# Kernel tuning notes

Hardware: AMD Instinct MI355X
Metric: run time of the kernel (lower is better)

The kernel has to match this reference:

```python
import jax, jax.numpy as jnp
import numpy as np

MIN_SIZE = 16.0
PH, PW, SCALE = 7, 7, 0.0625


def _context_anchor(rois, hh, hw):
    """rois: [N,5] (batch_idx,x1,y1,x2,y2). Returns [N*8,5] context boxes, col0 = 0 label."""
    N = rois.shape[0]
    x1, y1, x2, y2 = rois[:, 1], rois[:, 2], rois[:, 3], rois[:, 4]
    w, h = x2 - x1, y2 - y1
    k = jnp.arange(3, dtype=rois.dtype)
    sx = x1[:, None] + w[:, None] * (k - 0.5)  # x1 - w + w*k + w/2
    sy = y1[:, None] + h[:, None] * (k - 0.5)
    # np.meshgrid(shift_x, shift_y).ravel() is y-major
    cx = jnp.broadcast_to(sx[:, None, :], (N, 3, 3)).reshape(N, 9)
    cy = jnp.broadcast_to(sy[:, :, None], (N, 3, 3)).reshape(N, 9)
    boxes = jnp.stack([cx - w[:, None] / 4, cy - h[:, None] / 4,
                       cx + w[:, None] / 4, cy + h[:, None] / 4], -1)  # [N,9,4]
    bw = boxes[..., 2] - boxes[..., 0] + 1
    bh = boxes[..., 3] - boxes[..., 1] + 1
    invalid = ((boxes[..., 0] < 0) | (boxes[..., 1] < 0) |
               (boxes[..., 2] >= hw) | (boxes[..., 3] >= hh) |
               (bw < MIN_SIZE) | (bh < MIN_SIZE))
    boxes = jnp.where(invalid[..., None], rois[:, None, 1:5], boxes)
    boxes = boxes[:, jnp.array([0, 1, 2, 3, 5, 6, 7, 8]), :]  # drop center cell
    gt = boxes.reshape(N * 8, 4)  # K = 8N
    # IoU(all roi boxes, gt) with +1 pixel convention (bbox_overlaps_batch)
    A = rois[:, 1:5]
    aw, ah = A[:, 2] - A[:, 0] + 1, A[:, 3] - A[:, 1] + 1
    gw, gh = gt[:, 2] - gt[:, 0] + 1, gt[:, 3] - gt[:, 1] + 1
    iw = jnp.maximum(jnp.minimum(A[:, None, 2], gt[None, :, 2]) - jnp.maximum(A[:, None, 0], gt[None, :, 0]) + 1, 0)
    ih = jnp.maximum(jnp.minimum(A[:, None, 3], gt[None, :, 3]) - jnp.maximum(A[:, None, 1], gt[None, :, 1]) + 1, 0)
    inter = iw * ih
    ov = inter / ((aw * ah)[:, None] + (gw * gh)[None, :] - inter)  # [N,K]
    ov = jnp.where(((gw == 1) & (gh == 1))[None, :], 0.0, ov)
    ov = jnp.where(((aw == 1) & (ah == 1))[:, None], -1.0, ov)
    gt_max = ov.max(0)          # best overlap per gt box
    best = ov.argmax(0)         # index of best-matching roi (torch's `_`)
    labels = gt_max >= 0.3
    w_cell, h_cell = gt[:, 2] - gt[:, 0], gt[:, 3] - gt[:, 1]
    rw = jnp.where(labels, rois[best, 3] - rois[best, 1], 0.0)
    rh = jnp.where(labels, rois[best, 4] - rois[best, 2], 0.0)
    labels = (labels & ~(jnp.maximum(rw, rh) >= jnp.maximum(w_cell, h_cell))
                     & ~(jnp.minimum(rw, rh) < jnp.minimum(w_cell, h_cell) / 3))
    gt = jnp.where(labels[:, None], rois[best][:, 1:5], gt)
    # original zeroes labels at the end -> label column is all zeros
    return jnp.concatenate([jnp.zeros((N * 8, 1), rois.dtype), gt], -1)


def _roi_pool(features, boxes, ph, pw, scale):
    """Classic Caffe max RoIPool. Assumes batch_size==1 (all batch indices 0)."""
    _, C, H, W = features.shape
    f = features[0]  # [C,H,W]
    sw = jnp.round(boxes[:, 1] * scale)
    sh = jnp.round(boxes[:, 2] * scale)
    ew = jnp.round(boxes[:, 3] * scale)
    eh = jnp.round(boxes[:, 4] * scale)
    bsh = jnp.maximum(eh - sh + 1, 1.0) / ph
    bsw = jnp.maximum(ew - sw + 1, 1.0) / pw
    ii = jnp.arange(ph, dtype=f.dtype)
    jj = jnp.arange(pw, dtype=f.dtype)
    hs = jnp.clip(jnp.floor(ii[None, :] * bsh[:, None]) + sh[:, None], 0, H)   # [R,ph]
    he = jnp.clip(jnp.ceil((ii[None, :] + 1) * bsh[:, None]) + sh[:, None], 0, H)
    ws = jnp.clip(jnp.floor(jj[None, :] * bsw[:, None]) + sw[:, None], 0, W)   # [R,pw]
    we = jnp.clip(jnp.ceil((jj[None, :] + 1) * bsw[:, None]) + sw[:, None], 0, W)
    hidx = jnp.arange(H, dtype=f.dtype)
    widx = jnp.arange(W, dtype=f.dtype)
    mask_h = (hidx >= hs[..., None]) & (hidx < he[..., None])  # [R,ph,H]
    mask_w = (widx >= ws[..., None]) & (widx < we[..., None])  # [R,pw,W]
    NEG = jnp.asarray(-1e30, f.dtype)
    # separable masked max: reduce W per pw-bin, then H per ph-bin
    colmax = jnp.stack([jnp.where(mask_w[:, j, None, None, :], f[None], NEG).max(-1)
                        for j in range(pw)], axis=1)           # [R,pw,C,H]
    out = jnp.stack([jnp.where(mask_h[:, i, None, None, :], colmax, NEG).max(-1)
                     for i in range(ph)], axis=1)              # [R,ph,pw,C]
    valid = mask_h.any(-1)[:, :, None] & mask_w.any(-1)[:, None, :]
    out = jnp.where(valid[..., None], out, 0.0)                # empty bins -> 0
    return jnp.transpose(out, (0, 3, 1, 2))                    # [R,C,ph,pw]


def reference(features, rois, hh, hw):
    N = rois.shape[0]
    gt = _context_anchor(rois, hh, hw).reshape(N, 8, 5)
    cat_rois = jnp.concatenate([rois[:, None, :], gt], 1).reshape(-1, 5)  # [9N,5]
    pool = _roi_pool(features, cat_rois, PH, PW, SCALE)                   # [9N,C,7,7]
    pool_feat = pool.reshape(N, -1, PW, PH)                               # [N,9C,7,7]
    return pool_feat, cat_rois


def setup_inputs() -> dict:
    key = jax.random.key(0)
    k1, k2, k3, k4, k5 = jax.random.split(key, 5)
    N, C, Hf, Wf, IMG = 32, 256, 40, 40, 640
    x1 = jax.random.uniform(k1, (N,), minval=0.0, maxval=IMG - 220.0)
    y1 = jax.random.uniform(k2, (N,), minval=0.0, maxval=IMG - 220.0)
    bw = jax.random.uniform(k3, (N,), minval=80.0, maxval=200.0)
    bh = jax.random.uniform(k4, (N,), minval=80.0, maxval=200.0)
    rois = jnp.stack([jnp.zeros((N,)), x1, y1, x1 + bw, y1 + bh], -1).astype(jnp.float32)
    features = jax.random.normal(k5, (1, C, Hf, Wf), dtype=jnp.float32)
    return {"features": features, "rois": rois, "hh": 640, "hw": 640}
```

## Files before the change

### kernel.cpp

```cpp
#include <hip/hip_runtime.h>
#include <math.h>

#define N_ROIS   32
#define N_CAT    (N_ROIS * 9)
#define C_FEAT   256
#define H_FEAT   40
#define W_FEAT   40
#define P_FEAT   (H_FEAT * W_FEAT)
#define PH       7
#define PW       7
#define SCALE    0.0625f
#define MIN_SIZE 16.0f
#define CELLS    (PH * PW)
#define POOL_PER_BOX (C_FEAT * CELLS)
#define OUT_POOL_ELEMS ((size_t)N_CAT * POOL_PER_BOX)

#define N_TRANS_BLOCKS (P_FEAT / 32 * (C_FEAT / 32))
#define WIN 14

__global__ void prep_kernel(const float* __restrict__ f,
                            const float* __restrict__ rois,
                            const int* __restrict__ hh_p,
                            const int* __restrict__ hw_p,
                            float* __restrict__ ft,
                            float* __restrict__ cat_out,
                            int use_transpose) {
    __shared__ float tile[32][33];
    __shared__ float R[N_ROIS * 5];
    const int bid = blockIdx.x;
    const int tid = threadIdx.x;

    if (bid < N_TRANS_BLOCKS) {
        if (!use_transpose) return;
        const int pt = (bid % (P_FEAT / 32)) * 32;
        const int ct = (bid / (P_FEAT / 32)) * 32;
        const int lx = tid & 31;
        const int ly = tid >> 5;
        #pragma unroll
        for (int i = 0; i < 32; i += 8)
            tile[ly + i][lx] = f[(ct + ly + i) * P_FEAT + (pt + lx)];
        __syncthreads();
        #pragma unroll
        for (int i = 0; i < 32; i += 8)
            ft[(pt + ly + i) * C_FEAT + (ct + lx)] = tile[lx][ly + i];
        return;
    }

    if (tid < N_ROIS * 5) R[tid] = rois[tid];
    __syncthreads();

    const float hh = (float)(*hh_p);
    const float hw = (float)(*hw_p);

    const int g = tid;
    const int n = g >> 3;
    const int j = g & 7;
    const int m = (j < 4) ? j : j + 1;
    const int r  = m / 3;
    const int cc = m % 3;

    const float x1 = R[n * 5 + 1], y1 = R[n * 5 + 2];
    const float x2 = R[n * 5 + 3], y2 = R[n * 5 + 4];
    const float w = x2 - x1, h = y2 - y1;

    const float cx = x1 + w * ((float)cc - 0.5f);
    const float cy = y1 + h * ((float)r  - 0.5f);
    float bx1 = cx - w * 0.25f;
    float by1 = cy - h * 0.25f;
    float bx2 = cx + w * 0.25f;
    float by2 = cy + h * 0.25f;
    const float bw = bx2 - bx1 + 1.0f;
    const float bh = by2 - by1 + 1.0f;
    const bool invalid = (bx1 < 0.0f) || (by1 < 0.0f) ||
                         (bx2 >= hw) || (by2 >= hh) ||
                         (bw < MIN_SIZE) || (bh < MIN_SIZE);
    if (invalid) { bx1 = x1; by1 = y1; bx2 = x2; by2 = y2; }

    const float gw = bx2 - bx1 + 1.0f;
    const float gh = by2 - by1 + 1.0f;
    const float garea = gw * gh;
    const bool gdeg = (gw == 1.0f) && (gh == 1.0f);

    float best_ov = -INFINITY;
    int best = 0;
    for (int a = 0; a < N_ROIS; ++a) {
        const float ax1 = R[a * 5 + 1], ay1 = R[a * 5 + 2];
        const float ax2 = R[a * 5 + 3], ay2 = R[a * 5 + 4];
        const float aw = ax2 - ax1 + 1.0f, ah = ay2 - ay1 + 1.0f;
        float iw = fminf(ax2, bx2) - fmaxf(ax1, bx1) + 1.0f;
        float ih = fminf(ay2, by2) - fmaxf(ay1, by1) + 1.0f;
        iw = fmaxf(iw, 0.0f);
        ih = fmaxf(ih, 0.0f);
        const float inter = iw * ih;
        float ov = inter / (aw * ah + garea - inter);
        if (gdeg) ov = 0.0f;
        if (aw == 1.0f && ah == 1.0f) ov = -1.0f;
        if (ov > best_ov) { best_ov = ov; best = a; }
    }

    bool label = (best_ov >= 0.3f);
    const float w_cell = bx2 - bx1;
    const float h_cell = by2 - by1;
    const float rw = label ? (R[best * 5 + 3] - R[best * 5 + 1]) : 0.0f;
    const float rh = label ? (R[best * 5 + 4] - R[best * 5 + 2]) : 0.0f;
    label = label &&
            !(fmaxf(rw, rh) >= fmaxf(w_cell, h_cell)) &&
            !(fminf(rw, rh) < fminf(w_cell, h_cell) / 3.0f);
    if (label) {
        bx1 = R[best * 5 + 1]; by1 = R[best * 5 + 2];
        bx2 = R[best * 5 + 3]; by2 = R[best * 5 + 4];
    }

    float* row = cat_out + (size_t)(n * 9 + 1 + j) * 5;
    row[0] = 0.0f;
    row[1] = bx1; row[2] = by1; row[3] = bx2; row[4] = by2;
    if (j == 0) {
        float* rr = cat_out + (size_t)(n * 9) * 5;
        #pragma unroll
        for (int t = 0; t < 5; ++t) rr[t] = R[n * 5 + t];
    }
}

__global__ __launch_bounds__(256) void
roi_pool_kernel(const float* __restrict__ feat,
                const float* __restrict__ cat_rois,
                float* __restrict__ out) {
    const int i = blockIdx.x / N_CAT;
    const int b = blockIdx.x % N_CAT;
    const int c = threadIdx.x;

    const float* cr = cat_rois + (size_t)b * 5;
    const float x1 = cr[1], y1 = cr[2], x2 = cr[3], y2 = cr[4];
    const float sw = rintf(x1 * SCALE);
    const float sh = rintf(y1 * SCALE);
    const float ew = rintf(x2 * SCALE);
    const float eh = rintf(y2 * SCALE);
    const float bsh = fmaxf(eh - sh + 1.0f, 1.0f) * (1.0f / (float)PH);
    const float bsw = fmaxf(ew - sw + 1.0f, 1.0f) * (1.0f / (float)PW);

    const int hs = (int)fminf(fmaxf(floorf((float)i * bsh) + sh, 0.0f), (float)H_FEAT);
    const int he = (int)fminf(fmaxf(ceilf((float)(i + 1) * bsh) + sh, 0.0f), (float)H_FEAT);

    int ws[PW], we[PW];
    #pragma unroll
    for (int j = 0; j < PW; ++j) {
        ws[j] = (int)fminf(fmaxf(floorf((float)j * bsw) + sw, 0.0f), (float)W_FEAT);
        we[j] = (int)fminf(fmaxf(ceilf((float)(j + 1) * bsw) + sw, 0.0f), (float)W_FEAT);
    }

    const int xs = ws[0];
    const bool narrow = (bsw <= 2.0f);

    float mx[PW];
    #pragma unroll
    for (int j = 0; j < PW; ++j) mx[j] = -1e30f;

    if (narrow) {
        for (int y = hs; y < he; ++y) {
            const float* fr = feat + (size_t)(y * W_FEAT) * C_FEAT + c;
            float win[WIN];
            #pragma unroll
            for (int k = 0; k < WIN; ++k) {
                int x = xs + k;
                x = (x < W_FEAT - 1) ? x : (W_FEAT - 1);
                win[k] = fr[(size_t)x * C_FEAT];
            }
            #pragma unroll
            for (int j = 0; j < PW; ++j) {
                const int lo = ws[j], hi = we[j];
                const int kmax = (2 * j + 2 < WIN) ? (2 * j + 2) : WIN;
                #pragma unroll
                for (int k = 0; k < kmax; ++k) {
                    const int x = xs + k;
                    const bool in = (x >= lo) & (x < hi);
                    const float t = fmaxf(mx[j], win[k]);
                    mx[j] = in ? t : mx[j];
                }
            }
        }
    } else {
        for (int y = hs; y < he; ++y) {
            const float* fr = feat + (size_t)(y * W_FEAT) * C_FEAT + c;
            #pragma unroll
            for (int j = 0; j < PW; ++j)
                for (int x = ws[j]; x < we[j]; ++x)
                    mx[j] = fmaxf(mx[j], fr[(size_t)x * C_FEAT]);
        }
    }

    const bool rowv = (he > hs);
    float* ob = out + (size_t)b * POOL_PER_BOX + (size_t)c * CELLS + i * PW;
    #pragma unroll
    for (int j = 0; j < PW; ++j)
        ob[j] = (rowv && (we[j] > ws[j])) ? mx[j] : 0.0f;
}

__global__ __launch_bounds__(256) void
roi_pool_kernel_nchw(const float* __restrict__ feat,
                     const float* __restrict__ cat_rois,
                     float* __restrict__ out) {
    const int i = blockIdx.x / N_CAT;
    const int b = blockIdx.x % N_CAT;
    const int c = threadIdx.x;

    const float* cr = cat_rois + (size_t)b * 5;
    const float sw = rintf(cr[1] * SCALE);
    const float sh = rintf(cr[2] * SCALE);
    const float ew = rintf(cr[3] * SCALE);
    const float eh = rintf(cr[4] * SCALE);
    const float bsh = fmaxf(eh - sh + 1.0f, 1.0f) * (1.0f / (float)PH);
    const float bsw = fmaxf(ew - sw + 1.0f, 1.0f) * (1.0f / (float)PW);

    const int hs = (int)fminf(fmaxf(floorf((float)i * bsh) + sh, 0.0f), (float)H_FEAT);
    const int he = (int)fminf(fmaxf(ceilf((float)(i + 1) * bsh) + sh, 0.0f), (float)H_FEAT);
    int ws[PW], we[PW];
    #pragma unroll
    for (int j = 0; j < PW; ++j) {
        ws[j] = (int)fminf(fmaxf(floorf((float)j * bsw) + sw, 0.0f), (float)W_FEAT);
        we[j] = (int)fminf(fmaxf(ceilf((float)(j + 1) * bsw) + sw, 0.0f), (float)W_FEAT);
    }
    float mx[PW];
    #pragma unroll
    for (int j = 0; j < PW; ++j) mx[j] = -1e30f;
    for (int y = hs; y < he; ++y) {
        const float* fr = feat + (size_t)c * P_FEAT + y * W_FEAT;
        #pragma unroll
        for (int j = 0; j < PW; ++j)
            for (int x = ws[j]; x < we[j]; ++x)
                mx[j] = fmaxf(mx[j], fr[x]);
    }
    const bool rowv = (he > hs);
    float* ob = out + (size_t)b * POOL_PER_BOX + (size_t)c * CELLS + i * PW;
    #pragma unroll
    for (int j = 0; j < PW; ++j)
        ob[j] = (rowv && (we[j] > ws[j])) ? mx[j] : 0.0f;
}

extern "C" void kernel_launch(void* const* d_in, const int* in_sizes, int n_in,
                              void* d_out, int out_size, void* d_ws, size_t ws_size,
                              hipStream_t stream) {
    const float* features = (const float*)d_in[0];
    const float* rois     = (const float*)d_in[1];
    const int*   hh_p     = (const int*)d_in[2];
    const int*   hw_p     = (const int*)d_in[3];

    float* out      = (float*)d_out;
    float* cat_out  = out + OUT_POOL_ELEMS;
    float* ft       = (float*)d_ws;

    const size_t ft_bytes = (size_t)C_FEAT * P_FEAT * sizeof(float);
    const int use_transpose = (ws_size >= ft_bytes) ? 1 : 0;

    hipLaunchKernelGGL(prep_kernel, dim3(N_TRANS_BLOCKS + 1), dim3(256), 0, stream,
                       features, rois, hh_p, hw_p, ft, cat_out, use_transpose);

    if (use_transpose) {
        hipLaunchKernelGGL(roi_pool_kernel, dim3(PH * N_CAT), dim3(C_FEAT), 0, stream,
                           ft, cat_out, out);
    } else {
        hipLaunchKernelGGL(roi_pool_kernel_nchw, dim3(PH * N_CAT), dim3(C_FEAT), 0, stream,
                           features, cat_out, out);
    }
}
```

Before: 82.17 us.

## Pool whole box per block with shared-memory staging for coalesced float4 output

```diff
diff --git a/kernel.cpp b/kernel.cpp
--- a/kernel.cpp
+++ b/kernel.cpp
@@ -17,6 +17,10 @@
 
 #define N_TRANS_BLOCKS (P_FEAT / 32 * (C_FEAT / 32))
 #define WIN 14
+
+#define CH_HALF   128
+#define POOL_BLKS (N_CAT * 2)
+#define HALF_ELEMS (CH_HALF * CELLS)
 
 __global__ void prep_kernel(const float* __restrict__ f,
                             const float* __restrict__ rois,
@@ -121,13 +125,19 @@
     }
 }
 
-__global__ __launch_bounds__(256) void
-roi_pool_kernel(const float* __restrict__ feat,
+__global__ __launch_bounds__(512, 4) void
+pool_box_kernel(const float* __restrict__ feat,
                 const float* __restrict__ cat_rois,
                 float* __restrict__ out) {
-    const int i = blockIdx.x / N_CAT;
-    const int b = blockIdx.x % N_CAT;
-    const int c = threadIdx.x;
+    __shared__ __align__(16) float obuf[HALF_ELEMS];
+
+    const int s     = (blockIdx.x & 7) * (POOL_BLKS / 8) + (blockIdx.x >> 3);
+    const int b     = s >> 1;
+    const int chalf = s & 1;
+    const int tid   = threadIdx.x;
+    const int cl    = tid & (CH_HALF - 1);
+    const int c     = chalf * CH_HALF + cl;
+    const int iq    = tid >> 7;
 
     const float* cr = cat_rois + (size_t)b * 5;
     const float x1 = cr[1], y1 = cr[2], x2 = cr[3], y2 = cr[4];
@@ -138,9 +148,6 @@
     const float bsh = fmaxf(eh - sh + 1.0f, 1.0f) * (1.0f / (float)PH);
     const float bsw = fmaxf(ew - sw + 1.0f, 1.0f) * (1.0f / (float)PW);
 
-    const int hs = (int)fminf(fmaxf(floorf((float)i * bsh) + sh, 0.0f), (float)H_FEAT);
-    const int he = (int)fminf(fmaxf(ceilf((float)(i + 1) * bsh) + sh, 0.0f), (float)H_FEAT);
-
     int ws[PW], we[PW];
     #pragma unroll
     for (int j = 0; j < PW; ++j) {
@@ -151,48 +158,65 @@
     const int xs = ws[0];
     const bool narrow = (bsw <= 2.0f);
 
-    float mx[PW];
-    #pragma unroll
-    for (int j = 0; j < PW; ++j) mx[j] = -1e30f;
-
-    if (narrow) {
-        for (int y = hs; y < he; ++y) {
-            const float* fr = feat + (size_t)(y * W_FEAT) * C_FEAT + c;
-            float win[WIN];
-            #pragma unroll
-            for (int k = 0; k < WIN; ++k) {
-                int x = xs + k;
-                x = (x < W_FEAT - 1) ? x : (W_FEAT - 1);
-                win[k] = fr[(size_t)x * C_FEAT];
-            }
-            #pragma unroll
-            for (int j = 0; j < PW; ++j) {
-                const int lo = ws[j], hi = we[j];
-                const int kmax = (2 * j + 2 < WIN) ? (2 * j + 2) : WIN;
+    #pragma unroll
+    for (int ii = 0; ii < 2; ++ii) {
+        const int i = iq + ii * 4;
+        if (i >= PH) break;
+
+        const int hs = (int)fminf(fmaxf(floorf((float)i * bsh) + sh, 0.0f), (float)H_FEAT);
+        const int he = (int)fminf(fmaxf(ceilf((float)(i + 1) * bsh) + sh, 0.0f), (float)H_FEAT);
+
+        float mx[PW];
+        #pragma unroll
+        for (int j = 0; j < PW; ++j) mx[j] = -1e30f;
+
+        if (narrow) {
+            for (int y = hs; y < he; ++y) {
+                const float* fr = feat + (size_t)(y * W_FEAT) * C_FEAT + c;
+                float win[WIN];
                 #pragma unroll
-                for (int k = 0; k < kmax; ++k) {
-                    const int x = xs + k;
-                    const bool in = (x >= lo) & (x < hi);
-                    const float t = fmaxf(mx[j], win[k]);
-                    mx[j] = in ? t : mx[j];
+                for (int k = 0; k < WIN; ++k) {
+                    int x = xs + k;
+                    x = (x < W_FEAT - 1) ? x : (W_FEAT - 1);
+                    win[k] = fr[(size_t)x * C_FEAT];
+                }
+                #pragma unroll
+                for (int j = 0; j < PW; ++j) {
+                    const int lo = ws[j], hi = we[j];
+                    const int kmax = (2 * j + 2 < WIN) ? (2 * j + 2) : WIN;
+                    #pragma unroll
+                    for (int k = 0; k < kmax; ++k) {
+                        const int x = xs + k;
+                        const bool in = (x >= lo) & (x < hi);
+                        const float t = fmaxf(mx[j], win[k]);
+                        mx[j] = in ? t : mx[j];
+                    }
                 }
             }
+        } else {
+            for (int y = hs; y < he; ++y) {
+                const float* fr = feat + (size_t)(y * W_FEAT) * C_FEAT + c;
+                #pragma unroll
+                for (int j = 0; j < PW; ++j)
+                    for (int x = ws[j]; x < we[j]; ++x)
+                        mx[j] = fmaxf(mx[j], fr[(size_t)x * C_FEAT]);
+            }
         }
-    } else {
-        for (int y = hs; y < he; ++y) {
-            const float* fr = feat + (size_t)(y * W_FEAT) * C_FEAT + c;
-            #pragma unroll
-            for (int j = 0; j < PW; ++j)
-                for (int x = ws[j]; x < we[j]; ++x)
-                    mx[j] = fmaxf(mx[j], fr[(size_t)x * C_FEAT]);
-        }
-    }
-
-    const bool rowv = (he > hs);
-    float* ob = out + (size_t)b * POOL_PER_BOX + (size_t)c * CELLS + i * PW;
-    #pragma unroll
-    for (int j = 0; j < PW; ++j)
-        ob[j] = (rowv && (we[j] > ws[j])) ? mx[j] : 0.0f;
+
+        const bool rowv = (he > hs);
+        float* orow = obuf + cl * CELLS + i * PW;
+        #pragma unroll
+        for (int j = 0; j < PW; ++j)
+            orow[j] = (rowv && (we[j] > ws[j])) ? mx[j] : 0.0f;
+    }
+
+    __syncthreads();
+
+    const float4* src = reinterpret_cast<const float4*>(obuf);
+    float4* dst = reinterpret_cast<float4*>(out + (size_t)b * POOL_PER_BOX
+                                                + (size_t)chalf * HALF_ELEMS);
+    for (int e = tid; e < HALF_ELEMS / 4; e += 512)
+        dst[e] = src[e];
 }
 
 __global__ __launch_bounds__(256) void
@@ -255,7 +279,7 @@
                        features, rois, hh_p, hw_p, ft, cat_out, use_transpose);
 
     if (use_transpose) {
-        hipLaunchKernelGGL(roi_pool_kernel, dim3(PH * N_CAT), dim3(C_FEAT), 0, stream,
+        hipLaunchKernelGGL(pool_box_kernel, dim3(POOL_BLKS), dim3(512), 0, stream,
                            ft, cat_out, out);
     } else {
         hipLaunchKernelGGL(roi_pool_kernel_nchw, dim3(PH * N_CAT), dim3(C_FEAT), 0, stream,
```

New measurement: 86.12 us. 4.8% more time.

## Fuse anchor prep and ROI pooling into one kernel with shared-memory window

Applied to the files above, without the earlier changes.

```diff
diff --git a/kernel.cpp b/kernel.cpp
--- a/kernel.cpp
+++ b/kernel.cpp
@@ -15,176 +15,183 @@
 #define POOL_PER_BOX (C_FEAT * CELLS)
 #define OUT_POOL_ELEMS ((size_t)N_CAT * POOL_PER_BOX)
 
-#define N_TRANS_BLOCKS (P_FEAT / 32 * (C_FEAT / 32))
-#define WIN 14
-
-__global__ void prep_kernel(const float* __restrict__ f,
-                            const float* __restrict__ rois,
-                            const int* __restrict__ hh_p,
-                            const int* __restrict__ hw_p,
-                            float* __restrict__ ft,
-                            float* __restrict__ cat_out,
-                            int use_transpose) {
-    __shared__ float tile[32][33];
+#define CH_G      64
+#define NCHG      (C_FEAT / CH_G)
+#define POOL_BLKS (N_CAT * NCHG)
+#define THREADS   448
+#define WROWS     14
+#define WCOLS     14
+#define WSTRIDE   197
+
+__global__ __launch_bounds__(THREADS, 4) void
+fused_pool_kernel(const float* __restrict__ f,
+                  const float* __restrict__ rois,
+                  const int* __restrict__ hh_p,
+                  const int* __restrict__ hw_p,
+                  float* __restrict__ out) {
     __shared__ float R[N_ROIS * 5];
+    __shared__ float BX[4];
+    __shared__ __align__(16) float win[CH_G * WSTRIDE];
+
     const int bid = blockIdx.x;
+    const int s   = (bid & 7) * (POOL_BLKS / 8) + (bid >> 3);
+    const int b   = s >> 2;
+    const int cg  = s & 3;
     const int tid = threadIdx.x;
-
-    if (bid < N_TRANS_BLOCKS) {
-        if (!use_transpose) return;
-        const int pt = (bid % (P_FEAT / 32)) * 32;
-        const int ct = (bid / (P_FEAT / 32)) * 32;
-        const int lx = tid & 31;
-        const int ly = tid >> 5;
-        #pragma unroll
-        for (int i = 0; i < 32; i += 8)
-            tile[ly + i][lx] = f[(ct + ly + i) * P_FEAT + (pt + lx)];
-        __syncthreads();
-        #pragma unroll
-        for (int i = 0; i < 32; i += 8)
-            ft[(pt + ly + i) * C_FEAT + (ct + lx)] = tile[lx][ly + i];
-        return;
-    }
 
     if (tid < N_ROIS * 5) R[tid] = rois[tid];
     __syncthreads();
 
-    const float hh = (float)(*hh_p);
-    const float hw = (float)(*hw_p);
-
-    const int g = tid;
-    const int n = g >> 3;
-    const int j = g & 7;
-    const int m = (j < 4) ? j : j + 1;
-    const int r  = m / 3;
-    const int cc = m % 3;
-
-    const float x1 = R[n * 5 + 1], y1 = R[n * 5 + 2];
-    const float x2 = R[n * 5 + 3], y2 = R[n * 5 + 4];
-    const float w = x2 - x1, h = y2 - y1;
-
-    const float cx = x1 + w * ((float)cc - 0.5f);
-    const float cy = y1 + h * ((float)r  - 0.5f);
-    float bx1 = cx - w * 0.25f;
-    float by1 = cy - h * 0.25f;
-    float bx2 = cx + w * 0.25f;
-    float by2 = cy + h * 0.25f;
-    const float bw = bx2 - bx1 + 1.0f;
-    const float bh = by2 - by1 + 1.0f;
-    const bool invalid = (bx1 < 0.0f) || (by1 < 0.0f) ||
-                         (bx2 >= hw) || (by2 >= hh) ||
-                         (bw < MIN_SIZE) || (bh < MIN_SIZE);
-    if (invalid) { bx1 = x1; by1 = y1; bx2 = x2; by2 = y2; }
-
-    const float gw = bx2 - bx1 + 1.0f;
-    const float gh = by2 - by1 + 1.0f;
-    const float garea = gw * gh;
-    const bool gdeg = (gw == 1.0f) && (gh == 1.0f);
-
-    float best_ov = -INFINITY;
-    int best = 0;
-    for (int a = 0; a < N_ROIS; ++a) {
-        const float ax1 = R[a * 5 + 1], ay1 = R[a * 5 + 2];
-        const float ax2 = R[a * 5 + 3], ay2 = R[a * 5 + 4];
-        const float aw = ax2 - ax1 + 1.0f, ah = ay2 - ay1 + 1.0f;
-        float iw = fminf(ax2, bx2) - fmaxf(ax1, bx1) + 1.0f;
-        float ih = fminf(ay2, by2) - fmaxf(ay1, by1) + 1.0f;
-        iw = fmaxf(iw, 0.0f);
-        ih = fmaxf(ih, 0.0f);
-        const float inter = iw * ih;
-        float ov = inter / (aw * ah + garea - inter);
-        if (gdeg) ov = 0.0f;
-        if (aw == 1.0f && ah == 1.0f) ov = -1.0f;
-        if (ov > best_ov) { best_ov = ov; best = a; }
+    if (tid < 64) {
+        const int n  = b / 9;
+        const int jj = b % 9;
+        const float x1 = R[n * 5 + 1], y1 = R[n * 5 + 2];
+        const float x2 = R[n * 5 + 3], y2 = R[n * 5 + 4];
+        float bx1, by1, bx2, by2;
+
+        if (jj == 0) {
+            bx1 = x1; by1 = y1; bx2 = x2; by2 = y2;
+            if (tid == 0 && cg == 0) {
+                float* rr = out + OUT_POOL_ELEMS + (size_t)b * 5;
+                #pragma unroll
+                for (int t = 0; t < 5; ++t) rr[t] = R[n * 5 + t];
+            }
+        } else {
+            const int j = jj - 1;
+            const int m = (j < 4) ? j : j + 1;
+            const int r  = m / 3;
+            const int cc = m % 3;
+            const float w = x2 - x1, h = y2 - y1;
+            const float cx = x1 + w * ((float)cc - 0.5f);
+            const float cy = y1 + h * ((float)r  - 0.5f);
+            bx1 = cx - w * 0.25f;
+            by1 = cy - h * 0.25f;
+            bx2 = cx + w * 0.25f;
+            by2 = cy + h * 0.25f;
+            const float bw = bx2 - bx1 + 1.0f;
+            const float bh = by2 - by1 + 1.0f;
+            const float hh = (float)(*hh_p);
+            const float hw = (float)(*hw_p);
+            const bool invalid = (bx1 < 0.0f) || (by1 < 0.0f) ||
+                                 (bx2 >= hw) || (by2 >= hh) ||
+                                 (bw < MIN_SIZE) || (bh < MIN_SIZE);
+            if (invalid) { bx1 = x1; by1 = y1; bx2 = x2; by2 = y2; }
+
+            const float gw = bx2 - bx1 + 1.0f;
+            const float gh = by2 - by1 + 1.0f;
+            const float garea = gw * gh;
+            const bool gdeg = (gw == 1.0f) && (gh == 1.0f);
+
+            float best_ov = -INFINITY;
+            int best = 0;
+            for (int a = 0; a < N_ROIS; ++a) {
+                const float ax1 = R[a * 5 + 1], ay1 = R[a * 5 + 2];
+                const float ax2 = R[a * 5 + 3], ay2 = R[a * 5 + 4];
+                const float aw = ax2 - ax1 + 1.0f, ah = ay2 - ay1 + 1.0f;
+                float iw = fminf(ax2, bx2) - fmaxf(ax1, bx1) + 1.0f;
+                float ih = fminf(ay2, by2) - fmaxf(ay1, by1) + 1.0f;
+                iw = fmaxf(iw, 0.0f);
+                ih = fmaxf(ih, 0.0f);
+                const float inter = iw * ih;
+                float ov = inter / (aw * ah + garea - inter);
+                if (gdeg) ov = 0.0f;
+                if (aw == 1.0f && ah == 1.0f) ov = -1.0f;
+                if (ov > best_ov) { best_ov = ov; best = a; }
+            }
+
+            bool label = (best_ov >= 0.3f);
+            const float w_cell = bx2 - bx1;
+            const float h_cell = by2 - by1;
+            const float rw = label ? (R[best * 5 + 3] - R[best * 5 + 1]) : 0.0f;
+            const float rh = label ? (R[best * 5 + 4] - R[best * 5 + 2]) : 0.0f;
+            label = label &&
+                    !(fmaxf(rw, rh) >= fmaxf(w_cell, h_cell)) &&
+                    !(fminf(rw, rh) < fminf(w_cell, h_cell) / 3.0f);
+            if (label) {
+                bx1 = R[best * 5 + 1]; by1 = R[best * 5 + 2];
+                bx2 = R[best * 5 + 3]; by2 = R[best * 5 + 4];
+            }
+            if (tid == 0 && cg == 0) {
+                float* row = out + OUT_POOL_ELEMS + (size_t)b * 5;
+                row[0] = 0.0f;
+                row[1] = bx1; row[2] = by1; row[3] = bx2; row[4] = by2;
+            }
+        }
+        if (tid == 0) { BX[0] = bx1; BX[1] = by1; BX[2] = bx2; BX[3] = by2; }
     }
-
-    bool label = (best_ov >= 0.3f);
-    const float w_cell = bx2 - bx1;
-    const float h_cell = by2 - by1;
-    const float rw = label ? (R[best * 5 + 3] - R[best * 5 + 1]) : 0.0f;
-    const float rh = label ? (R[best * 5 + 4] - R[best * 5 + 2]) : 0.0f;
-    label = label &&
-            !(fmaxf(rw, rh) >= fmaxf(w_cell, h_cell)) &&
-            !(fminf(rw, rh) < fminf(w_cell, h_cell) / 3.0f);
-    if (label) {
-        bx1 = R[best * 5 + 1]; by1 = R[best * 5 + 2];
-        bx2 = R[best * 5 + 3]; by2 = R[best * 5 + 4];
-    }
-
-    float* row = cat_out + (size_t)(n * 9 + 1 + j) * 5;
-    row[0] = 0.0f;
-    row[1] = bx1; row[2] = by1; row[3] = bx2; row[4] = by2;
-    if (j == 0) {
-        float* rr = cat_out + (size_t)(n * 9) * 5;
-        #pragma unroll
-        for (int t = 0; t < 5; ++t) rr[t] = R[n * 5 + t];
-    }
-}
-
-__global__ __launch_bounds__(256) void
-roi_pool_kernel(const float* __restrict__ feat,
-                const float* __restrict__ cat_rois,
-                float* __restrict__ out) {
-    const int i = blockIdx.x / N_CAT;
-    const int b = blockIdx.x % N_CAT;
-    const int c = threadIdx.x;
-
-    const float* cr = cat_rois + (size_t)b * 5;
-    const float x1 = cr[1], y1 = cr[2], x2 = cr[3], y2 = cr[4];
-    const float sw = rintf(x1 * SCALE);
-    const float sh = rintf(y1 * SCALE);
-    const float ew = rintf(x2 * SCALE);
-    const float eh = rintf(y2 * SCALE);
+    __syncthreads();
+
+    const float bx1 = BX[0], by1 = BX[1], bx2 = BX[2], by2 = BX[3];
+
+    const float sw = rintf(bx1 * SCALE);
+    const float sh = rintf(by1 * SCALE);
+    const float ew = rintf(bx2 * SCALE);
+    const float eh = rintf(by2 * SCALE);
     const float bsh = fmaxf(eh - sh + 1.0f, 1.0f) * (1.0f / (float)PH);
     const float bsw = fmaxf(ew - sw + 1.0f, 1.0f) * (1.0f / (float)PW);
 
+    int wsA[PW], weA[PW];
+    #pragma unroll
+    for (int j = 0; j < PW; ++j) {
+        wsA[j] = (int)fminf(fmaxf(floorf((float)j * bsw) + sw, 0.0f), (float)W_FEAT);
+        weA[j] = (int)fminf(fmaxf(ceilf((float)(j + 1) * bsw) + sw, 0.0f), (float)W_FEAT);
+    }
+    const int xs = wsA[0];
+    const int ys = (int)fminf(fmaxf(sh, 0.0f), (float)H_FEAT);
+
+    const int cl = tid & 63;
+    const int i  = tid >> 6;
+    const int c  = cg * CH_G + cl;
+
     const int hs = (int)fminf(fmaxf(floorf((float)i * bsh) + sh, 0.0f), (float)H_FEAT);
     const int he = (int)fminf(fmaxf(ceilf((float)(i + 1) * bsh) + sh, 0.0f), (float)H_FEAT);
 
-    int ws[PW], we[PW];
-    #pragma unroll
-    for (int j = 0; j < PW; ++j) {
-        ws[j] = (int)fminf(fmaxf(floorf((float)j * bsw) + sw, 0.0f), (float)W_FEAT);
-        we[j] = (int)fminf(fmaxf(ceilf((float)(j + 1) * bsw) + sw, 0.0f), (float)W_FEAT);
-    }
-
-    const int xs = ws[0];
-    const bool narrow = (bsw <= 2.0f);
+    const bool narrow = (bsw <= 2.0f) && (bsh <= 2.0f);
 
     float mx[PW];
     #pragma unroll
     for (int j = 0; j < PW; ++j) mx[j] = -1e30f;
 
     if (narrow) {
+        #pragma unroll 4
+        for (int e = tid; e < CH_G * WROWS * WCOLS; e += THREADS) {
+            const int ch = e / (WROWS * WCOLS);
+            const int p  = e - ch * (WROWS * WCOLS);
+            const int yy = p / WCOLS;
+            const int xx = p - yy * WCOLS;
+            const int gy = (ys + yy < H_FEAT - 1) ? (ys + yy) : (H_FEAT - 1);
+            const int gx = (xs + xx < W_FEAT - 1) ? (xs + xx) : (W_FEAT - 1);
+            win[ch * WSTRIDE + p] =
+                f[(size_t)(cg * CH_G + ch) * P_FEAT + gy * W_FEAT + gx];
+        }
+        __syncthreads();
+
         for (int y = hs; y < he; ++y) {
-            const float* fr = feat + (size_t)(y * W_FEAT) * C_FEAT + c;
-            float win[WIN];
+            const int ly = y - ys;
+            const float* wr = win + cl * WSTRIDE + ly * WCOLS;
+            float wk[WCOLS];
             #pragma unroll
-            for (int k = 0; k < WIN; ++k) {
-                int x = xs + k;
-                x = (x < W_FEAT - 1) ? x : (W_FEAT - 1);
-                win[k] = fr[(size_t)x * C_FEAT];
-            }
+            for (int k = 0; k < WCOLS; ++k) wk[k] = wr[k];
             #pragma unroll
             for (int j = 0; j < PW; ++j) {
-                const int lo = ws[j], hi = we[j];
-                const int kmax = (2 * j + 2 < WIN) ? (2 * j + 2) : WIN;
+                const int lo = wsA[j], hi = weA[j];
+                const int kmax = (2 * j + 2 < WCOLS) ? (2 * j + 2) : WCOLS;
                 #pragma unroll
                 for (int k = 0; k < kmax; ++k) {
                     const int x = xs + k;
                     const bool in = (x >= lo) & (x < hi);
-                    const float t = fmaxf(mx[j], win[k]);
+                    const float t = fmaxf(mx[j], wk[k]);
                     mx[j] = in ? t : mx[j];
                 }
             }
         }
     } else {
         for (int y = hs; y < he; ++y) {
-            const float* fr = feat + (size_t)(y * W_FEAT) * C_FEAT + c;
+            const float* fr = f + (size_t)c * P_FEAT + y * W_FEAT;
             #pragma unroll
             for (int j = 0; j < PW; ++j)
-                for (int x = ws[j]; x < we[j]; ++x)
-                    mx[j] = fmaxf(mx[j], fr[(size_t)x * C_FEAT]);
+                for (int x = wsA[j]; x < weA[j]; ++x)
+                    mx[j] = fmaxf(mx[j], fr[x]);
         }
     }
 
@@ -192,48 +199,7 @@
     float* ob = out + (size_t)b * POOL_PER_BOX + (size_t)c * CELLS + i * PW;
     #pragma unroll
     for (int j = 0; j < PW; ++j)
-        ob[j] = (rowv && (we[j] > ws[j])) ? mx[j] : 0.0f;
-}
-
-__global__ __launch_bounds__(256) void
-roi_pool_kernel_nchw(const float* __restrict__ feat,
-                     const float* __restrict__ cat_rois,
-                     float* __restrict__ out) {
-    const int i = blockIdx.x / N_CAT;
-    const int b = blockIdx.x % N_CAT;
-    const int c = threadIdx.x;
-
-    const float* cr = cat_rois + (size_t)b * 5;
-    const float sw = rintf(cr[1] * SCALE);
-    const float sh = rintf(cr[2] * SCALE);
-    const float ew = rintf(cr[3] * SCALE);
-    const float eh = rintf(cr[4] * SCALE);
-    const float bsh = fmaxf(eh - sh + 1.0f, 1.0f) * (1.0f / (float)PH);
-    const float bsw = fmaxf(ew - sw + 1.0f, 1.0f) * (1.0f / (float)PW);
-
-    const int hs = (int)fminf(fmaxf(floorf((float)i * bsh) + sh, 0.0f), (float)H_FEAT);
-    const int he = (int)fminf(fmaxf(ceilf((float)(i + 1) * bsh) + sh, 0.0f), (float)H_FEAT);
-    int ws[PW], we[PW];
-    #pragma unroll
-    for (int j = 0; j < PW; ++j) {
-        ws[j] = (int)fminf(fmaxf(floorf((float)j * bsw) + sw, 0.0f), (float)W_FEAT);
-        we[j] = (int)fminf(fmaxf(ceilf((float)(j + 1) * bsw) + sw, 0.0f), (float)W_FEAT);
-    }
-    float mx[PW];
-    #pragma unroll
-    for (int j = 0; j < PW; ++j) mx[j] = -1e30f;
-    for (int y = hs; y < he; ++y) {
-        const float* fr = feat + (size_t)c * P_FEAT + y * W_FEAT;
-        #pragma unroll
-        for (int j = 0; j < PW; ++j)
-            for (int x = ws[j]; x < we[j]; ++x)
-                mx[j] = fmaxf(mx[j], fr[x]);
-    }
-    const bool rowv = (he > hs);
-    float* ob = out + (size_t)b * POOL_PER_BOX + (size_t)c * CELLS + i * PW;
-    #pragma unroll
-    for (int j = 0; j < PW; ++j)
-        ob[j] = (rowv && (we[j] > ws[j])) ? mx[j] : 0.0f;
+        ob[j] = (rowv && (weA[j] > wsA[j])) ? mx[j] : 0.0f;
 }
 
 extern "C" void kernel_launch(void* const* d_in, const int* in_sizes, int n_in,
@@ -244,21 +210,9 @@
     const int*   hh_p     = (const int*)d_in[2];
     const int*   hw_p     = (const int*)d_in[3];
 
-    float* out      = (float*)d_out;
-    float* cat_out  = out + OUT_POOL_ELEMS;
-    float* ft       = (float*)d_ws;
-
-    const size_t ft_bytes = (size_t)C_FEAT * P_FEAT * sizeof(float);
-    const int use_transpose = (ws_size >= ft_bytes) ? 1 : 0;
-
-    hipLaunchKernelGGL(prep_kernel, dim3(N_TRANS_BLOCKS + 1), dim3(256), 0, stream,
-                       features, rois, hh_p, hw_p, ft, cat_out, use_transpose);
-
-    if (use_transpose) {
-        hipLaunchKernelGGL(roi_pool_kernel, dim3(PH * N_CAT), dim3(C_FEAT), 0, stream,
-                           ft, cat_out, out);
-    } else {
-        hipLaunchKernelGGL(roi_pool_kernel_nchw, dim3(PH * N_CAT), dim3(C_FEAT), 0, stream,
-                           features, cat_out, out);
-    }
+    float* out = (float*)d_out;
+    (void)d_ws; (void)ws_size; (void)in_sizes; (void)n_in; (void)out_size;
+
+    hipLaunchKernelGGL(fused_pool_kernel, dim3(POOL_BLKS), dim3(THREADS), 0, stream,
+                       features, rois, hh_p, hw_p, out);
 }
```

Measured after the change: 100.7 us. 1.23x slower.

## Vectorize ROI pool over channels with float4 and single-wavefront blocks

Applied to the files above, without the earlier changes.

```diff
diff --git a/kernel.cpp b/kernel.cpp
--- a/kernel.cpp
+++ b/kernel.cpp
@@ -16,7 +16,7 @@
 #define OUT_POOL_ELEMS ((size_t)N_CAT * POOL_PER_BOX)
 
 #define N_TRANS_BLOCKS (P_FEAT / 32 * (C_FEAT / 32))
-#define WIN 14
+#define CQ (C_FEAT / 4)
 
 __global__ void prep_kernel(const float* __restrict__ f,
                             const float* __restrict__ rois,
@@ -121,13 +121,13 @@
     }
 }
 
-__global__ __launch_bounds__(256) void
-roi_pool_kernel(const float* __restrict__ feat,
-                const float* __restrict__ cat_rois,
-                float* __restrict__ out) {
+__global__ __launch_bounds__(64) void
+roi_pool_v3(const float* __restrict__ ft,
+            const float* __restrict__ cat_rois,
+            float* __restrict__ out) {
     const int i = blockIdx.x / N_CAT;
     const int b = blockIdx.x % N_CAT;
-    const int c = threadIdx.x;
+    const int l = threadIdx.x;
 
     const float* cr = cat_rois + (size_t)b * 5;
     const float x1 = cr[1], y1 = cr[2], x2 = cr[3], y2 = cr[4];
@@ -138,61 +138,50 @@
     const float bsh = fmaxf(eh - sh + 1.0f, 1.0f) * (1.0f / (float)PH);
     const float bsw = fmaxf(ew - sw + 1.0f, 1.0f) * (1.0f / (float)PW);
 
-    const int hs = (int)fminf(fmaxf(floorf((float)i * bsh) + sh, 0.0f), (float)H_FEAT);
-    const int he = (int)fminf(fmaxf(ceilf((float)(i + 1) * bsh) + sh, 0.0f), (float)H_FEAT);
+    const int hs = __builtin_amdgcn_readfirstlane(
+        (int)fminf(fmaxf(floorf((float)i * bsh) + sh, 0.0f), (float)H_FEAT));
+    const int he = __builtin_amdgcn_readfirstlane(
+        (int)fminf(fmaxf(ceilf((float)(i + 1) * bsh) + sh, 0.0f), (float)H_FEAT));
 
     int ws[PW], we[PW];
     #pragma unroll
     for (int j = 0; j < PW; ++j) {
-        ws[j] = (int)fminf(fmaxf(floorf((float)j * bsw) + sw, 0.0f), (float)W_FEAT);
-        we[j] = (int)fminf(fmaxf(ceilf((float)(j + 1) * bsw) + sw, 0.0f), (float)W_FEAT);
-    }
-
-    const int xs = ws[0];
-    const bool narrow = (bsw <= 2.0f);
-
-    float mx[PW];
-    #pragma unroll
-    for (int j = 0; j < PW; ++j) mx[j] = -1e30f;
-
-    if (narrow) {
-        for (int y = hs; y < he; ++y) {
-            const float* fr = feat + (size_t)(y * W_FEAT) * C_FEAT + c;
-            float win[WIN];
-            #pragma unroll
-            for (int k = 0; k < WIN; ++k) {
-                int x = xs + k;
-                x = (x < W_FEAT - 1) ? x : (W_FEAT - 1);
-                win[k] = fr[(size_t)x * C_FEAT];
-            }
-            #pragma unroll
-            for (int j = 0; j < PW; ++j) {
-                const int lo = ws[j], hi = we[j];
-                const int kmax = (2 * j + 2 < WIN) ? (2 * j + 2) : WIN;
-                #pragma unroll
-                for (int k = 0; k < kmax; ++k) {
-                    const int x = xs + k;
-                    const bool in = (x >= lo) & (x < hi);
-                    const float t = fmaxf(mx[j], win[k]);
-                    mx[j] = in ? t : mx[j];
-                }
+        ws[j] = __builtin_amdgcn_readfirstlane(
+            (int)fminf(fmaxf(floorf((float)j * bsw) + sw, 0.0f), (float)W_FEAT));
+        we[j] = __builtin_amdgcn_readfirstlane(
+            (int)fminf(fmaxf(ceilf((float)(j + 1) * bsw) + sw, 0.0f), (float)W_FEAT));
+    }
+
+    float4 mx[PW];
+    #pragma unroll
+    for (int j = 0; j < PW; ++j)
+        mx[j] = make_float4(-1e30f, -1e30f, -1e30f, -1e30f);
+
+    for (int y = hs; y < he; ++y) {
+        const float4* py = (const float4*)ft + (size_t)(y * W_FEAT) * CQ + l;
+        #pragma unroll
+        for (int j = 0; j < PW; ++j) {
+            for (int x = ws[j]; x < we[j]; ++x) {
+                const float4 v = py[(size_t)x * CQ];
+                mx[j].x = fmaxf(mx[j].x, v.x);
+                mx[j].y = fmaxf(mx[j].y, v.y);
+                mx[j].z = fmaxf(mx[j].z, v.z);
+                mx[j].w = fmaxf(mx[j].w, v.w);
             }
         }
-    } else {
-        for (int y = hs; y < he; ++y) {
-            const float* fr = feat + (size_t)(y * W_FEAT) * C_FEAT + c;
-            #pragma unroll
-            for (int j = 0; j < PW; ++j)
-                for (int x = ws[j]; x < we[j]; ++x)
-                    mx[j] = fmaxf(mx[j], fr[(size_t)x * C_FEAT]);
-        }
     }
 
     const bool rowv = (he > hs);
-    float* ob = out + (size_t)b * POOL_PER_BOX + (size_t)c * CELLS + i * PW;
-    #pragma unroll
-    for (int j = 0; j < PW; ++j)
-        ob[j] = (rowv && (we[j] > ws[j])) ? mx[j] : 0.0f;
+    float* ob = out + (size_t)b * POOL_PER_BOX + (size_t)(4 * l) * CELLS + i * PW;
+    #pragma unroll
+    for (int j = 0; j < PW; ++j) {
+        const bool val = rowv && (we[j] > ws[j]);
+        const float4 m = mx[j];
+        ob[j]             = val ? m.x : 0.0f;
+        ob[j + CELLS]     = val ? m.y : 0.0f;
+        ob[j + 2 * CELLS] = val ? m.z : 0.0f;
+        ob[j + 3 * CELLS] = val ? m.w : 0.0f;
+    }
 }
 
 __global__ __launch_bounds__(256) void
@@ -255,7 +244,7 @@
                        features, rois, hh_p, hw_p, ft, cat_out, use_transpose);
 
     if (use_transpose) {
-        hipLaunchKernelGGL(roi_pool_kernel, dim3(PH * N_CAT), dim3(C_FEAT), 0, stream,
+        hipLaunchKernelGGL(roi_pool_v3, dim3(PH * N_CAT), dim3(64), 0, stream,
                            ft, cat_out, out);
     } else {
         hipLaunchKernelGGL(roi_pool_kernel_nchw, dim3(PH * N_CAT), dim3(C_FEAT), 0, stream,
```

New measurement: 85.09 us. 3.6% more time.
